# Optimization experiments

Hardware: AMD Instinct MI355X
Metric: run time of the kernel (lower is better)

The kernel has to match this reference:

```python
import jax, jax.numpy as jnp
import numpy as np

B, H = 8192, 768


def _mk_linear(key, fan_in, fan_out):
    k1, k2 = jax.random.split(key)
    lim = 1.0 / np.sqrt(fan_in)
    W = jax.random.uniform(k1, (fan_out, fan_in), jnp.float32, -lim, lim)
    b = jax.random.uniform(k2, (fan_out,), jnp.float32, -lim, lim)
    return W, b


def setup_inputs() -> dict:
    key = jax.random.key(0)
    ks = jax.random.split(key, 6)
    modal_a = jax.random.normal(ks[0], (B, H), jnp.float32)
    modal_b = jax.random.normal(ks[1], (B, H), jnp.float32)
    W1m, b1m = _mk_linear(ks[2], H, H)
    W2m, b2m = _mk_linear(ks[3], H, H)
    W1v, b1v = _mk_linear(ks[4], H, H)
    W2v, b2v = _mk_linear(ks[5], H, H)
    return {"modal_a": modal_a, "modal_b": modal_b,
            "W1m": W1m, "b1m": b1m, "W2m": W2m, "b2m": b2m,
            "W1v": W1v, "b1v": b1v, "W2v": W2v, "b2v": b2v}


def reference(modal_a, modal_b, W1m, b1m, W2m, b2m, W1v, b1v, W2v, b2v):
    # mlp_mu: Linear -> Tanh -> Linear
    mu = jnp.tanh(modal_a @ W1m.T + b1m) @ W2m.T + b2m              # [B,H]
    # mlp_logvar: Linear -> Tanh -> Linear -> Tanh
    logvar = jnp.tanh(jnp.tanh(modal_a @ W1v.T + b1v) @ W2v.T + b2v)  # [B,H]
    inv_var = jnp.exp(-logvar)

    positive = -(mu - modal_b) ** 2 * 0.5 * inv_var                  # [B,H]

    # mean_j (mu[j] - mu[i])^2 = E[mu^2] - 2*mu[i]*E[mu] + mu[i]^2  (per feature dim)
    # Algebraic reduction of the O(B^2*H) tile in the original code.
    mu_mean = jnp.mean(mu, axis=0)                                   # [H]
    mu_sq_mean = jnp.mean(mu * mu, axis=0)                           # [H]
    pair_sq = mu_sq_mean - 2.0 * mu * mu_mean + mu * mu              # [B,H]
    negative = -pair_sq * 0.5 * inv_var                              # [B,H]

    pos_sum = jnp.sum(positive, axis=-1)                             # [B]
    neg_sum = jnp.sum(negative, axis=-1)                             # [B]
    lld = jnp.mean(pos_sum)
    bound = jnp.mean(pos_sum - neg_sum)
    return (lld, bound)
```

## Files before the change

### kernel.cpp

```cpp
#include <hip/hip_runtime.h>
#include <hip/hip_fp8.h>
#include <math.h>

typedef float v4f __attribute__((ext_vector_type(4)));

static constexpr int Bn = 8192;
static constexpr int Hn = 768;
static constexpr float invB = 1.0f / 8192.0f;

__device__ __forceinline__ unsigned char cvt_e4m3(float x) {
    __hip_fp8_e4m3 t(x);
    return t.__x;
}

__device__ __forceinline__ float fast_tanh(float x) {
    float xc = fminf(fmaxf(x, -15.0f), 15.0f);
    float e = __expf(2.0f * xc);
    float r = __builtin_amdgcn_rcpf(e + 1.0f);
    return 1.0f - 2.0f * r;
}

__global__ void prep_kernel(const float* __restrict__ A,
                            const float* __restrict__ W1m, const float* __restrict__ W2m,
                            const float* __restrict__ W1v, const float* __restrict__ W2v,
                            unsigned char* __restrict__ A_f8,
                            unsigned char* __restrict__ W1m_f8, unsigned char* __restrict__ W2m_f8,
                            unsigned char* __restrict__ W1v_f8, unsigned char* __restrict__ W2v_f8,
                            float* __restrict__ zbuf, int nzero) {
    const int tid = blockIdx.x * blockDim.x + threadIdx.x;
    if (tid < nzero) zbuf[tid] = 0.0f;
    constexpr int A4 = Bn * Hn / 4;
    constexpr int W4 = Hn * Hn / 4;
    const int total = A4 + 4 * W4;
    const int stride = gridDim.x * blockDim.x;
    for (int i = tid; i < total; i += stride) {
        const float* s; unsigned char* d; int j;
        if (i < A4) { s = A; d = A_f8; j = i; }
        else {
            int k = i - A4; int w = k / W4; j = k - w * W4;
            s = (w == 0) ? W1m : (w == 1) ? W2m : (w == 2) ? W1v : W2v;
            d = (w == 0) ? W1m_f8 : (w == 1) ? W2m_f8 : (w == 2) ? W1v_f8 : W2v_f8;
        }
        float4 v = ((const float4*)s)[j];
        unsigned p = (unsigned)cvt_e4m3(v.x)
                   | ((unsigned)cvt_e4m3(v.y) << 8)
                   | ((unsigned)cvt_e4m3(v.z) << 16)
                   | ((unsigned)cvt_e4m3(v.w) << 24);
        ((unsigned*)d)[j] = p;
    }
}


__launch_bounds__(512, 2)
__global__ void gemm_l1(const unsigned char* __restrict__ A_g,
                        const unsigned char* __restrict__ Wm_g, const unsigned char* __restrict__ Wv_g,
                        const float* __restrict__ bm, const float* __restrict__ bv,
                        unsigned char* __restrict__ outm, unsigned char* __restrict__ outv) {
    __shared__ __align__(16) unsigned char As[64 * 768];
    const int t = threadIdx.x;
    const int strip0 = blockIdx.x * 64;
    const int br = blockIdx.y;
    const unsigned char* __restrict__ Wg = br ? Wv_g : Wm_g;
    const float* __restrict__ bias = br ? bv : bm;
    unsigned char* __restrict__ out = br ? outv : outm;

    {
        const int row = t >> 3, c8 = t & 7;
        const unsigned char* src = A_g + (size_t)(strip0 + row) * Hn + c8 * 16;
        unsigned char* dst = As + row * 768;
#pragma unroll
        for (int j = 0; j < 6; ++j) {
            const int c = c8 + 8 * j;
            uint4 v = *(const uint4*)(src + j * 128);
            *(uint4*)(dst + ((c ^ (row & 7)) << 4)) = v;
        }
    }
    __syncthreads();

    const int w = t >> 6, lane = t & 63;
    const int lr = lane & 15, quad = lane >> 4;
    const int wc0 = w * 96;

    const unsigned char* __restrict__ pW = Wg + (size_t)(wc0 + lr) * Hn + quad * 16;

    v4f acc[6][4] = {};
    ulonglong2 Wf[2][6], Af[2][4];

#define L1_LOADS(s_, ms_) do {                                                              \
    _Pragma("unroll")                                                                       \
    for (int ct = 0; ct < 6; ++ct)                                                          \
        Wf[s_][ct] = *(const ulonglong2*)(pW + ct * (16 * Hn) + (ms_) * 64);                \
    _Pragma("unroll")                                                                       \
    for (int rt = 0; rt < 4; ++rt) {                                                        \
        const int row_ = rt * 16 + lr;                                                      \
        const int slot_ = ((ms_) * 4 + quad) ^ (row_ & 7);                                  \
        Af[s_][rt] = *(const ulonglong2*)&As[row_ * 768 + slot_ * 16];                      \
    } } while (0)

#define L1_MFMA(s_) do {                                                                    \
    _Pragma("unroll")                                                                       \
    for (int ct = 0; ct < 6; ++ct)                                                          \
    _Pragma("unroll")                                                                       \
    for (int rt = 0; rt < 4; ++rt) {                                                        \
        acc[ct][rt] = __builtin_amdgcn_mfma_f32_16x16x32_fp8_fp8((long)Wf[s_][ct].x, (long)Af[s_][rt].x, acc[ct][rt], 0, 0, 0); \
        acc[ct][rt] = __builtin_amdgcn_mfma_f32_16x16x32_fp8_fp8((long)Wf[s_][ct].y, (long)Af[s_][rt].y, acc[ct][rt], 0, 0, 0); \
    } } while (0)

    L1_LOADS(0, 0);
#pragma unroll
    for (int ms = 0; ms < 12; ++ms) {
        if (ms < 11) {
            if ((ms & 1) == 0) L1_LOADS(1, ms + 1); else L1_LOADS(0, ms + 1);
        }
        if ((ms & 1) == 0) L1_MFMA(0); else L1_MFMA(1);
    }
#undef L1_LOADS
#undef L1_MFMA

    __syncthreads();
#pragma unroll
    for (int ct = 0; ct < 6; ++ct) {
        const float4 bb = *(const float4*)&bias[wc0 + ct * 16 + quad * 4];
        const int c = w * 6 + ct;
#pragma unroll
        for (int rt = 0; rt < 4; ++rt) {
            const int row = rt * 16 + lr;
            v4f a = acc[ct][rt];
            unsigned p = (unsigned)cvt_e4m3(fast_tanh(a[0] + bb.x))
                       | ((unsigned)cvt_e4m3(fast_tanh(a[1] + bb.y)) << 8)
                       | ((unsigned)cvt_e4m3(fast_tanh(a[2] + bb.z)) << 16)
                       | ((unsigned)cvt_e4m3(fast_tanh(a[3] + bb.w)) << 24);
            *(unsigned*)&As[row * 768 + ((c ^ (row & 7)) << 4) + quad * 4] = p;
        }
    }
    __syncthreads();
#pragma unroll
    for (int i = 0; i < 6; ++i) {
        const int u = i * 512 + t;
        const int row = u / 48, c = u - row * 48;
        uint4 v = *(const uint4*)&As[row * 768 + ((c ^ (row & 7)) << 4)];
        *(uint4*)&out[(size_t)(strip0 + row) * Hn + c * 16] = v;
    }
}

__device__ __forceinline__ void l2_gemm(const unsigned char* Hsrc, const unsigned char* pW,
                                        int lr, int quad, v4f acc[2][6]) {
    ulonglong2 Wf[2][6], Af[2][2];
#define L2_LOADS(s_, ms_) do {                                                              \
    _Pragma("unroll")                                                                       \
    for (int ct = 0; ct < 6; ++ct)                                                          \
        Wf[s_][ct] = *(const ulonglong2*)(pW + ct * (16 * Hn) + (ms_) * 64);                \
    _Pragma("unroll")                                                                       \
    for (int rt = 0; rt < 2; ++rt) {                                                        \
        const int row_ = rt * 16 + lr;                                                      \
        const int slot_ = ((ms_) * 4 + quad) ^ (row_ & 7);                                  \
        Af[s_][rt] = *(const ulonglong2*)&Hsrc[row_ * 768 + slot_ * 16];                    \
    } } while (0)

#define L2_MFMA(s_) do {                                                                    \
    _Pragma("unroll")                                                                       \
    for (int rt = 0; rt < 2; ++rt)                                                          \
    _Pragma("unroll")                                                                       \
    for (int ct = 0; ct < 6; ++ct) {                                                        \
        acc[rt][ct] = __builtin_amdgcn_mfma_f32_16x16x32_fp8_fp8((long)Af[s_][rt].x, (long)Wf[s_][ct].x, acc[rt][ct], 0, 0, 0); \
        acc[rt][ct] = __builtin_amdgcn_mfma_f32_16x16x32_fp8_fp8((long)Af[s_][rt].y, (long)Wf[s_][ct].y, acc[rt][ct], 0, 0, 0); \
    } } while (0)

    L2_LOADS(0, 0);
#pragma unroll
    for (int ms = 0; ms < 12; ++ms) {
        if (ms < 11) {
            if ((ms & 1) == 0) L2_LOADS(1, ms + 1); else L2_LOADS(0, ms + 1);
        }
        if ((ms & 1) == 0) L2_MFMA(0); else L2_MFMA(1);
    }
#undef L2_LOADS
#undef L2_MFMA
}

__launch_bounds__(512, 2)
__global__ void gemm_l2(const unsigned char* __restrict__ h1m_g, const unsigned char* __restrict__ h1v_g,
                        const unsigned char* __restrict__ Wm_g, const unsigned char* __restrict__ Wv_g,
                        const float* __restrict__ bm, const float* __restrict__ bv,
                        const float* __restrict__ mb,
                        float* __restrict__ cs, float* __restrict__ cs2,
                        float* __restrict__ siv, float* __restrict__ sivmu,
                        float* __restrict__ accum, float* __restrict__ outp) {
    __shared__ __align__(16) unsigned char Hs[2][32 * 768];
    const int t = threadIdx.x;
    const int strip0 = blockIdx.x * 32;

    {
        const int row = t >> 4, c16 = t & 15;
        const size_t goff = (size_t)(strip0 + row) * Hn + c16 * 16;
#pragma unroll
        for (int b = 0; b < 2; ++b) {
            const unsigned char* src = (b ? h1v_g : h1m_g) + goff;
            unsigned char* dst = Hs[b] + row * 768;
#pragma unroll
            for (int j = 0; j < 3; ++j) {
                const int c = c16 + 16 * j;
                uint4 v = *(const uint4*)(src + j * 256);
                *(uint4*)(dst + ((c ^ (row & 7)) << 4)) = v;
            }
        }
    }
    __syncthreads();

    const int w = t >> 6, lane = t & 63;
    const int lr = lane & 15, quad = lane >> 4;
    const int wc0 = w * 96;

    v4f am[2][6] = {}, av[2][6] = {};

    l2_gemm(&Hs[0][0], Wm_g + (size_t)(wc0 + lr) * Hn + quad * 16, lr, quad, am);
    l2_gemm(&Hs[1][0], Wv_g + (size_t)(wc0 + lr) * Hn + quad * 16, lr, quad, av);

    float pos = 0.f, q = 0.f;
#pragma unroll
    for (int ct = 0; ct < 6; ++ct) {
        const int col = wc0 + ct * 16 + lr;
        const float bmc = bm[col], bvc = bv[col];
        float c1 = 0.f, c2 = 0.f, c3 = 0.f, c4 = 0.f;
#pragma unroll
        for (int rt = 0; rt < 2; ++rt) {
#pragma unroll
            for (int r = 0; r < 4; ++r) {
                const int row = strip0 + rt * 16 + quad * 4 + r;
                float mu = am[rt][ct][r] + bmc;
                float tv = fast_tanh(av[rt][ct][r] + bvc);
                float iv = __expf(-tv);
                float mbv = mb[(size_t)row * Hn + col];
                float d = mu - mbv;
                pos += iv * d * d;
                q   += iv * mu * mu;
                c1 += mu; c2 += mu * mu; c3 += iv; c4 += iv * mu;
            }
        }
        c1 += __shfl_xor(c1, 16); c1 += __shfl_xor(c1, 32);
        c2 += __shfl_xor(c2, 16); c2 += __shfl_xor(c2, 32);
        c3 += __shfl_xor(c3, 16); c3 += __shfl_xor(c3, 32);
        c4 += __shfl_xor(c4, 16); c4 += __shfl_xor(c4, 32);
        if (quad == 0) {
            atomicAdd(&cs[col], c1);
            atomicAdd(&cs2[col], c2);
            atomicAdd(&siv[col], c3);
            atomicAdd(&sivmu[col], c4);
        }
    }
    for (int off = 32; off > 0; off >>= 1) {
        pos += __shfl_down(pos, off);
        q   += __shfl_down(q, off);
    }
    __shared__ float redP[8], redQ[8];
    if (lane == 0) { redP[w] = pos; redQ[w] = q; }
    __syncthreads();
    __shared__ int is_last;
    if (t == 0) {
        float sp = 0.f, sq = 0.f;
#pragma unroll
        for (int i = 0; i < 8; ++i) { sp += redP[i]; sq += redQ[i]; }
        atomicAdd(&accum[0], sp);
        atomicAdd(&accum[1], sq);
        __threadfence();
        unsigned old = atomicAdd((unsigned int*)&accum[3], 1u);
        is_last = (old == gridDim.x * gridDim.y - 1) ? 1 : 0;
    }
    __syncthreads();
    if (is_last) {
        float term = 0.f;
        for (int h = t; h < Hn; h += 512) {
            float v1 = atomicAdd(&cs[h], 0.0f);
            float v2 = atomicAdd(&cs2[h], 0.0f);
            float v3 = atomicAdd(&siv[h], 0.0f);
            float v4 = atomicAdd(&sivmu[h], 0.0f);
            term += v3 * v2 - 2.0f * v4 * v1;
        }
        for (int off = 32; off > 0; off >>= 1) term += __shfl_down(term, off);
        __shared__ float redT[8];
        if (lane == 0) redT[w] = term;
        __syncthreads();
        if (t == 0) {
            float T = 0.f;
#pragma unroll
            for (int i = 0; i < 8; ++i) T += redT[i];
            float P = atomicAdd(&accum[0], 0.0f);
            float Q = atomicAdd(&accum[1], 0.0f);
            float pos_sum = -0.5f * P;
            float neg_sum = -0.5f * (T * invB + Q);
            outp[0] = pos_sum * invB;
            outp[1] = (pos_sum - neg_sum) * invB;
        }
    }
}

extern "C" void kernel_launch(void* const* d_in, const int* in_sizes, int n_in,
                              void* d_out, int out_size, void* d_ws, size_t ws_size,
                              hipStream_t stream) {
    const float* modal_a = (const float*)d_in[0];
    const float* modal_b = (const float*)d_in[1];
    const float* W1m = (const float*)d_in[2];
    const float* b1m = (const float*)d_in[3];
    const float* W2m = (const float*)d_in[4];
    const float* b2m = (const float*)d_in[5];
    const float* W1v = (const float*)d_in[6];
    const float* b1v = (const float*)d_in[7];
    const float* W2v = (const float*)d_in[8];
    const float* b2v = (const float*)d_in[9];
    float* out = (float*)d_out;

    char* ws = (char*)d_ws;
    constexpr size_t szA8 = (size_t)Bn * Hn;
    constexpr size_t szW8 = (size_t)Hn * Hn;
    unsigned char* A_f8   = (unsigned char*)(ws);
    unsigned char* h1m_f8 = (unsigned char*)(ws + szA8);
    unsigned char* h1v_f8 = (unsigned char*)(ws + 2 * szA8);
    unsigned char* W1m_f8 = (unsigned char*)(ws + 3 * szA8);
    unsigned char* W2m_f8 = (unsigned char*)(ws + 3 * szA8 + szW8);
    unsigned char* W1v_f8 = (unsigned char*)(ws + 3 * szA8 + 2 * szW8);
    unsigned char* W2v_f8 = (unsigned char*)(ws + 3 * szA8 + 3 * szW8);
    float* cs     = (float*)(ws + 3 * szA8 + 4 * szW8);
    float* cs2    = cs + Hn;
    float* siv    = cs + 2 * Hn;
    float* sivmu  = cs + 3 * Hn;
    float* accum  = cs + 4 * Hn;

    prep_kernel<<<1280, 256, 0, stream>>>(modal_a, W1m, W2m, W1v, W2v,
                                          A_f8, W1m_f8, W2m_f8, W1v_f8, W2v_f8,
                                          cs, 4 * Hn + 8);

    gemm_l1<<<dim3(Bn / 64, 2), 512, 0, stream>>>(
        A_f8, W1m_f8, W1v_f8, b1m, b1v, h1m_f8, h1v_f8);

    gemm_l2<<<dim3(Bn / 32), 512, 0, stream>>>(
        h1m_f8, h1v_f8, W2m_f8, W2v_f8, b2m, b2v, modal_b,
        cs, cs2, siv, sivmu, accum, out);
}
```

Before: 190.2 us.

## Fuse both MLP layers and input FP8 conversion into one kernel per row strip

Merges the layer-1 GEMM, the layer-2 GEMM and the epilogue into a single kernel working on 32-row strips. The fp32 input is converted to FP8 directly into shared memory and the hidden activations stay in shared memory, so the FP8 copy of A and the h1 round trips through global memory are gone. The mu and logvar branches now share each A fragment load. The prep kernel only converts weights. In exchange each block reloads all four weight matrices, holds more accumulator registers, and uses a wider 16-way XOR swizzle.

Measured after the change: 189.9 us. Within noise of the previous version (-0.1%).

```diff
diff --git a/kernel.cpp b/kernel.cpp
--- a/kernel.cpp
+++ b/kernel.cpp
@@ -11,6 +11,13 @@
 __device__ __forceinline__ unsigned char cvt_e4m3(float x) {
     __hip_fp8_e4m3 t(x);
     return t.__x;
+}
+
+__device__ __forceinline__ unsigned pack4_e4m3(float4 f) {
+    return (unsigned)cvt_e4m3(f.x)
+         | ((unsigned)cvt_e4m3(f.y) << 8)
+         | ((unsigned)cvt_e4m3(f.z) << 16)
+         | ((unsigned)cvt_e4m3(f.w) << 24);
 }
 
 __device__ __forceinline__ float fast_tanh(float x) {
@@ -20,59 +27,54 @@
     return 1.0f - 2.0f * r;
 }
 
-__global__ void prep_kernel(const float* __restrict__ A,
-                            const float* __restrict__ W1m, const float* __restrict__ W2m,
-                            const float* __restrict__ W1v, const float* __restrict__ W2v,
-                            unsigned char* __restrict__ A_f8,
-                            unsigned char* __restrict__ W1m_f8, unsigned char* __restrict__ W2m_f8,
-                            unsigned char* __restrict__ W1v_f8, unsigned char* __restrict__ W2v_f8,
-                            float* __restrict__ zbuf, int nzero) {
+__global__ void prep_w(const float* __restrict__ W1m, const float* __restrict__ W2m,
+                       const float* __restrict__ W1v, const float* __restrict__ W2v,
+                       unsigned char* __restrict__ W1m_f8, unsigned char* __restrict__ W2m_f8,
+                       unsigned char* __restrict__ W1v_f8, unsigned char* __restrict__ W2v_f8,
+                       float* __restrict__ zbuf, int nzero) {
     const int tid = blockIdx.x * blockDim.x + threadIdx.x;
     if (tid < nzero) zbuf[tid] = 0.0f;
-    constexpr int A4 = Bn * Hn / 4;
     constexpr int W4 = Hn * Hn / 4;
-    const int total = A4 + 4 * W4;
+    const int total = 4 * W4;
     const int stride = gridDim.x * blockDim.x;
     for (int i = tid; i < total; i += stride) {
-        const float* s; unsigned char* d; int j;
-        if (i < A4) { s = A; d = A_f8; j = i; }
-        else {
-            int k = i - A4; int w = k / W4; j = k - w * W4;
-            s = (w == 0) ? W1m : (w == 1) ? W2m : (w == 2) ? W1v : W2v;
-            d = (w == 0) ? W1m_f8 : (w == 1) ? W2m_f8 : (w == 2) ? W1v_f8 : W2v_f8;
-        }
+        int w = i / W4, j = i - w * W4;
+        const float* s = (w == 0) ? W1m : (w == 1) ? W2m : (w == 2) ? W1v : W2v;
+        unsigned char* d = (w == 0) ? W1m_f8 : (w == 1) ? W2m_f8 : (w == 2) ? W1v_f8 : W2v_f8;
         float4 v = ((const float4*)s)[j];
-        unsigned p = (unsigned)cvt_e4m3(v.x)
-                   | ((unsigned)cvt_e4m3(v.y) << 8)
-                   | ((unsigned)cvt_e4m3(v.z) << 16)
-                   | ((unsigned)cvt_e4m3(v.w) << 24);
-        ((unsigned*)d)[j] = p;
-    }
-}
-
+        ((unsigned*)d)[j] = pack4_e4m3(v);
+    }
+}
 
 __launch_bounds__(512, 2)
-__global__ void gemm_l1(const unsigned char* __restrict__ A_g,
-                        const unsigned char* __restrict__ Wm_g, const unsigned char* __restrict__ Wv_g,
-                        const float* __restrict__ bm, const float* __restrict__ bv,
-                        unsigned char* __restrict__ outm, unsigned char* __restrict__ outv) {
-    __shared__ __align__(16) unsigned char As[64 * 768];
+__global__ void club_fused(const float* __restrict__ A_g,
+                           const unsigned char* __restrict__ W1m, const unsigned char* __restrict__ W1v,
+                           const unsigned char* __restrict__ W2m, const unsigned char* __restrict__ W2v,
+                           const float* __restrict__ b1m, const float* __restrict__ b1v,
+                           const float* __restrict__ b2m, const float* __restrict__ b2v,
+                           const float* __restrict__ mb,
+                           float* __restrict__ cs, float* __restrict__ cs2,
+                           float* __restrict__ siv, float* __restrict__ sivmu,
+                           float* __restrict__ accum, float* __restrict__ outp) {
+    __shared__ __align__(16) unsigned char Hm[32 * 768];
+    __shared__ __align__(16) unsigned char Xs[32 * 768];
     const int t = threadIdx.x;
-    const int strip0 = blockIdx.x * 64;
-    const int br = blockIdx.y;
-    const unsigned char* __restrict__ Wg = br ? Wv_g : Wm_g;
-    const float* __restrict__ bias = br ? bv : bm;
-    unsigned char* __restrict__ out = br ? outv : outm;
+    const int strip0 = blockIdx.x * 32;
 
     {
-        const int row = t >> 3, c8 = t & 7;
-        const unsigned char* src = A_g + (size_t)(strip0 + row) * Hn + c8 * 16;
-        unsigned char* dst = As + row * 768;
-#pragma unroll
-        for (int j = 0; j < 6; ++j) {
-            const int c = c8 + 8 * j;
-            uint4 v = *(const uint4*)(src + j * 128);
-            *(uint4*)(dst + ((c ^ (row & 7)) << 4)) = v;
+        const int row = t >> 4, seg = t & 15;
+        const float* src = A_g + (size_t)(strip0 + row) * Hn;
+#pragma unroll
+        for (int j = 0; j < 3; ++j) {
+            const int c = seg + 16 * j;
+            float4 f0 = *(const float4*)(src + c * 16 + 0);
+            float4 f1 = *(const float4*)(src + c * 16 + 4);
+            float4 f2 = *(const float4*)(src + c * 16 + 8);
+            float4 f3 = *(const float4*)(src + c * 16 + 12);
+            uint4 p;
+            p.x = pack4_e4m3(f0); p.y = pack4_e4m3(f1);
+            p.z = pack4_e4m3(f2); p.w = pack4_e4m3(f3);
+            *(uint4*)&Xs[row * 768 + ((c ^ (row & 15)) << 4)] = p;
         }
     }
     __syncthreads();
@@ -81,154 +83,132 @@
     const int lr = lane & 15, quad = lane >> 4;
     const int wc0 = w * 96;
 
-    const unsigned char* __restrict__ pW = Wg + (size_t)(wc0 + lr) * Hn + quad * 16;
-
-    v4f acc[6][4] = {};
-    ulonglong2 Wf[2][6], Af[2][4];
-
-#define L1_LOADS(s_, ms_) do {                                                              \
-    _Pragma("unroll")                                                                       \
-    for (int ct = 0; ct < 6; ++ct)                                                          \
-        Wf[s_][ct] = *(const ulonglong2*)(pW + ct * (16 * Hn) + (ms_) * 64);                \
-    _Pragma("unroll")                                                                       \
-    for (int rt = 0; rt < 4; ++rt) {                                                        \
-        const int row_ = rt * 16 + lr;                                                      \
-        const int slot_ = ((ms_) * 4 + quad) ^ (row_ & 7);                                  \
-        Af[s_][rt] = *(const ulonglong2*)&As[row_ * 768 + slot_ * 16];                      \
+    v4f am[6][2] = {}, av[6][2] = {};
+    {
+        ulonglong2 Wm1[2][6], Wv1[2][6];
+        const unsigned char* __restrict__ pWm = W1m + (size_t)(wc0 + lr) * Hn + quad * 16;
+        const unsigned char* __restrict__ pWv = W1v + (size_t)(wc0 + lr) * Hn + quad * 16;
+
+#define LDW1(s_, ms_) do {                                                                  \
+    _Pragma("unroll")                                                                       \
+    for (int ct = 0; ct < 6; ++ct) {                                                        \
+        Wm1[s_][ct] = *(const ulonglong2*)(pWm + ct * (16 * Hn) + (ms_) * 64);              \
+        Wv1[s_][ct] = *(const ulonglong2*)(pWv + ct * (16 * Hn) + (ms_) * 64);              \
     } } while (0)
 
-#define L1_MFMA(s_) do {                                                                    \
-    _Pragma("unroll")                                                                       \
-    for (int ct = 0; ct < 6; ++ct)                                                          \
-    _Pragma("unroll")                                                                       \
-    for (int rt = 0; rt < 4; ++rt) {                                                        \
-        acc[ct][rt] = __builtin_amdgcn_mfma_f32_16x16x32_fp8_fp8((long)Wf[s_][ct].x, (long)Af[s_][rt].x, acc[ct][rt], 0, 0, 0); \
-        acc[ct][rt] = __builtin_amdgcn_mfma_f32_16x16x32_fp8_fp8((long)Wf[s_][ct].y, (long)Af[s_][rt].y, acc[ct][rt], 0, 0, 0); \
-    } } while (0)
-
-    L1_LOADS(0, 0);
-#pragma unroll
-    for (int ms = 0; ms < 12; ++ms) {
-        if (ms < 11) {
-            if ((ms & 1) == 0) L1_LOADS(1, ms + 1); else L1_LOADS(0, ms + 1);
-        }
-        if ((ms & 1) == 0) L1_MFMA(0); else L1_MFMA(1);
-    }
-#undef L1_LOADS
-#undef L1_MFMA
-
-    __syncthreads();
-#pragma unroll
-    for (int ct = 0; ct < 6; ++ct) {
-        const float4 bb = *(const float4*)&bias[wc0 + ct * 16 + quad * 4];
-        const int c = w * 6 + ct;
-#pragma unroll
-        for (int rt = 0; rt < 4; ++rt) {
-            const int row = rt * 16 + lr;
-            v4f a = acc[ct][rt];
-            unsigned p = (unsigned)cvt_e4m3(fast_tanh(a[0] + bb.x))
-                       | ((unsigned)cvt_e4m3(fast_tanh(a[1] + bb.y)) << 8)
-                       | ((unsigned)cvt_e4m3(fast_tanh(a[2] + bb.z)) << 16)
-                       | ((unsigned)cvt_e4m3(fast_tanh(a[3] + bb.w)) << 24);
-            *(unsigned*)&As[row * 768 + ((c ^ (row & 7)) << 4) + quad * 4] = p;
-        }
-    }
-    __syncthreads();
-#pragma unroll
-    for (int i = 0; i < 6; ++i) {
-        const int u = i * 512 + t;
-        const int row = u / 48, c = u - row * 48;
-        uint4 v = *(const uint4*)&As[row * 768 + ((c ^ (row & 7)) << 4)];
-        *(uint4*)&out[(size_t)(strip0 + row) * Hn + c * 16] = v;
-    }
-}
-
-__device__ __forceinline__ void l2_gemm(const unsigned char* Hsrc, const unsigned char* pW,
-                                        int lr, int quad, v4f acc[2][6]) {
-    ulonglong2 Wf[2][6], Af[2][2];
-#define L2_LOADS(s_, ms_) do {                                                              \
-    _Pragma("unroll")                                                                       \
-    for (int ct = 0; ct < 6; ++ct)                                                          \
-        Wf[s_][ct] = *(const ulonglong2*)(pW + ct * (16 * Hn) + (ms_) * 64);                \
+#define FM1(s_, ms_) do {                                                                   \
+    ulonglong2 Af[2];                                                                       \
     _Pragma("unroll")                                                                       \
     for (int rt = 0; rt < 2; ++rt) {                                                        \
         const int row_ = rt * 16 + lr;                                                      \
-        const int slot_ = ((ms_) * 4 + quad) ^ (row_ & 7);                                  \
-        Af[s_][rt] = *(const ulonglong2*)&Hsrc[row_ * 768 + slot_ * 16];                    \
+        const int k_ = (ms_) * 4 + quad;                                                    \
+        Af[rt] = *(const ulonglong2*)&Xs[row_ * 768 + ((k_ ^ (row_ & 15)) << 4)];           \
+    }                                                                                       \
+    _Pragma("unroll")                                                                       \
+    for (int ct = 0; ct < 6; ++ct)                                                          \
+    _Pragma("unroll")                                                                       \
+    for (int rt = 0; rt < 2; ++rt) {                                                        \
+        am[ct][rt] = __builtin_amdgcn_mfma_f32_16x16x32_fp8_fp8((long)Wm1[s_][ct].x, (long)Af[rt].x, am[ct][rt], 0, 0, 0); \
+        am[ct][rt] = __builtin_amdgcn_mfma_f32_16x16x32_fp8_fp8((long)Wm1[s_][ct].y, (long)Af[rt].y, am[ct][rt], 0, 0, 0); \
+        av[ct][rt] = __builtin_amdgcn_mfma_f32_16x16x32_fp8_fp8((long)Wv1[s_][ct].x, (long)Af[rt].x, av[ct][rt], 0, 0, 0); \
+        av[ct][rt] = __builtin_amdgcn_mfma_f32_16x16x32_fp8_fp8((long)Wv1[s_][ct].y, (long)Af[rt].y, av[ct][rt], 0, 0, 0); \
     } } while (0)
 
-#define L2_MFMA(s_) do {                                                                    \
+        LDW1(0, 0);
+#pragma unroll
+        for (int ms = 0; ms < 11; ++ms) {
+            if ((ms & 1) == 0) { LDW1(1, ms + 1); FM1(0, ms); }
+            else               { LDW1(0, ms + 1); FM1(1, ms); }
+        }
+        FM1(1, 11);
+#undef LDW1
+#undef FM1
+    }
+
+    __syncthreads();
+
+#pragma unroll
+    for (int ct = 0; ct < 6; ++ct) {
+        const float4 bbm = *(const float4*)&b1m[wc0 + ct * 16 + quad * 4];
+        const float4 bbv = *(const float4*)&b1v[wc0 + ct * 16 + quad * 4];
+        const int cc = w * 6 + ct;
+#pragma unroll
+        for (int rt = 0; rt < 2; ++rt) {
+            const int row = rt * 16 + lr;
+            v4f a = am[ct][rt];
+            unsigned pm = (unsigned)cvt_e4m3(fast_tanh(a[0] + bbm.x))
+                        | ((unsigned)cvt_e4m3(fast_tanh(a[1] + bbm.y)) << 8)
+                        | ((unsigned)cvt_e4m3(fast_tanh(a[2] + bbm.z)) << 16)
+                        | ((unsigned)cvt_e4m3(fast_tanh(a[3] + bbm.w)) << 24);
+            v4f b = av[ct][rt];
+            unsigned pv = (unsigned)cvt_e4m3(fast_tanh(b[0] + bbv.x))
+                        | ((unsigned)cvt_e4m3(fast_tanh(b[1] + bbv.y)) << 8)
+                        | ((unsigned)cvt_e4m3(fast_tanh(b[2] + bbv.z)) << 16)
+                        | ((unsigned)cvt_e4m3(fast_tanh(b[3] + bbv.w)) << 24);
+            const int off = row * 768 + ((cc ^ (row & 15)) << 4) + quad * 4;
+            *(unsigned*)&Hm[off] = pm;
+            *(unsigned*)&Xs[off] = pv;
+        }
+    }
+    __syncthreads();
+
+    v4f cm[2][6] = {}, cv[2][6] = {};
+    {
+        ulonglong2 Wm2[2][6], Wv2[2][6];
+        const unsigned char* __restrict__ pWm = W2m + (size_t)(wc0 + lr) * Hn + quad * 16;
+        const unsigned char* __restrict__ pWv = W2v + (size_t)(wc0 + lr) * Hn + quad * 16;
+
+#define LDW2(s_, ms_) do {                                                                  \
+    _Pragma("unroll")                                                                       \
+    for (int ct = 0; ct < 6; ++ct) {                                                        \
+        Wm2[s_][ct] = *(const ulonglong2*)(pWm + ct * (16 * Hn) + (ms_) * 64);              \
+        Wv2[s_][ct] = *(const ulonglong2*)(pWv + ct * (16 * Hn) + (ms_) * 64);              \
+    } } while (0)
+
+#define FM2(s_, ms_) do {                                                                   \
+    ulonglong2 Am[2], Av[2];                                                                \
+    _Pragma("unroll")                                                                       \
+    for (int rt = 0; rt < 2; ++rt) {                                                        \
+        const int row_ = rt * 16 + lr;                                                      \
+        const int k_ = (ms_) * 4 + quad;                                                    \
+        const int off_ = row_ * 768 + ((k_ ^ (row_ & 15)) << 4);                            \
+        Am[rt] = *(const ulonglong2*)&Hm[off_];                                             \
+        Av[rt] = *(const ulonglong2*)&Xs[off_];                                             \
+    }                                                                                       \
     _Pragma("unroll")                                                                       \
     for (int rt = 0; rt < 2; ++rt)                                                          \
     _Pragma("unroll")                                                                       \
     for (int ct = 0; ct < 6; ++ct) {                                                        \
-        acc[rt][ct] = __builtin_amdgcn_mfma_f32_16x16x32_fp8_fp8((long)Af[s_][rt].x, (long)Wf[s_][ct].x, acc[rt][ct], 0, 0, 0); \
-        acc[rt][ct] = __builtin_amdgcn_mfma_f32_16x16x32_fp8_fp8((long)Af[s_][rt].y, (long)Wf[s_][ct].y, acc[rt][ct], 0, 0, 0); \
+        cm[rt][ct] = __builtin_amdgcn_mfma_f32_16x16x32_fp8_fp8((long)Am[rt].x, (long)Wm2[s_][ct].x, cm[rt][ct], 0, 0, 0); \
+        cm[rt][ct] = __builtin_amdgcn_mfma_f32_16x16x32_fp8_fp8((long)Am[rt].y, (long)Wm2[s_][ct].y, cm[rt][ct], 0, 0, 0); \
+        cv[rt][ct] = __builtin_amdgcn_mfma_f32_16x16x32_fp8_fp8((long)Av[rt].x, (long)Wv2[s_][ct].x, cv[rt][ct], 0, 0, 0); \
+        cv[rt][ct] = __builtin_amdgcn_mfma_f32_16x16x32_fp8_fp8((long)Av[rt].y, (long)Wv2[s_][ct].y, cv[rt][ct], 0, 0, 0); \
     } } while (0)
 
-    L2_LOADS(0, 0);
-#pragma unroll
-    for (int ms = 0; ms < 12; ++ms) {
-        if (ms < 11) {
-            if ((ms & 1) == 0) L2_LOADS(1, ms + 1); else L2_LOADS(0, ms + 1);
-        }
-        if ((ms & 1) == 0) L2_MFMA(0); else L2_MFMA(1);
-    }
-#undef L2_LOADS
-#undef L2_MFMA
-}
-
-__launch_bounds__(512, 2)
-__global__ void gemm_l2(const unsigned char* __restrict__ h1m_g, const unsigned char* __restrict__ h1v_g,
-                        const unsigned char* __restrict__ Wm_g, const unsigned char* __restrict__ Wv_g,
-                        const float* __restrict__ bm, const float* __restrict__ bv,
-                        const float* __restrict__ mb,
-                        float* __restrict__ cs, float* __restrict__ cs2,
-                        float* __restrict__ siv, float* __restrict__ sivmu,
-                        float* __restrict__ accum, float* __restrict__ outp) {
-    __shared__ __align__(16) unsigned char Hs[2][32 * 768];
-    const int t = threadIdx.x;
-    const int strip0 = blockIdx.x * 32;
-
-    {
-        const int row = t >> 4, c16 = t & 15;
-        const size_t goff = (size_t)(strip0 + row) * Hn + c16 * 16;
-#pragma unroll
-        for (int b = 0; b < 2; ++b) {
-            const unsigned char* src = (b ? h1v_g : h1m_g) + goff;
-            unsigned char* dst = Hs[b] + row * 768;
-#pragma unroll
-            for (int j = 0; j < 3; ++j) {
-                const int c = c16 + 16 * j;
-                uint4 v = *(const uint4*)(src + j * 256);
-                *(uint4*)(dst + ((c ^ (row & 7)) << 4)) = v;
-            }
-        }
-    }
-    __syncthreads();
-
-    const int w = t >> 6, lane = t & 63;
-    const int lr = lane & 15, quad = lane >> 4;
-    const int wc0 = w * 96;
-
-    v4f am[2][6] = {}, av[2][6] = {};
-
-    l2_gemm(&Hs[0][0], Wm_g + (size_t)(wc0 + lr) * Hn + quad * 16, lr, quad, am);
-    l2_gemm(&Hs[1][0], Wv_g + (size_t)(wc0 + lr) * Hn + quad * 16, lr, quad, av);
+        LDW2(0, 0);
+#pragma unroll
+        for (int ms = 0; ms < 11; ++ms) {
+            if ((ms & 1) == 0) { LDW2(1, ms + 1); FM2(0, ms); }
+            else               { LDW2(0, ms + 1); FM2(1, ms); }
+        }
+        FM2(1, 11);
+#undef LDW2
+#undef FM2
+    }
 
     float pos = 0.f, q = 0.f;
 #pragma unroll
     for (int ct = 0; ct < 6; ++ct) {
         const int col = wc0 + ct * 16 + lr;
-        const float bmc = bm[col], bvc = bv[col];
+        const float bmc = b2m[col], bvc = b2v[col];
         float c1 = 0.f, c2 = 0.f, c3 = 0.f, c4 = 0.f;
 #pragma unroll
         for (int rt = 0; rt < 2; ++rt) {
 #pragma unroll
             for (int r = 0; r < 4; ++r) {
                 const int row = strip0 + rt * 16 + quad * 4 + r;
-                float mu = am[rt][ct][r] + bmc;
-                float tv = fast_tanh(av[rt][ct][r] + bvc);
+                float mu = cm[rt][ct][r] + bmc;
+                float tv = fast_tanh(cv[rt][ct][r] + bvc);
                 float iv = __expf(-tv);
                 float mbv = mb[(size_t)row * Hn + col];
                 float d = mu - mbv;
@@ -264,7 +244,7 @@
         atomicAdd(&accum[1], sq);
         __threadfence();
         unsigned old = atomicAdd((unsigned int*)&accum[3], 1u);
-        is_last = (old == gridDim.x * gridDim.y - 1) ? 1 : 0;
+        is_last = (old == gridDim.x - 1) ? 1 : 0;
     }
     __syncthreads();
     if (is_last) {
@@ -310,29 +290,23 @@
     float* out = (float*)d_out;
 
     char* ws = (char*)d_ws;
-    constexpr size_t szA8 = (size_t)Bn * Hn;
     constexpr size_t szW8 = (size_t)Hn * Hn;
-    unsigned char* A_f8   = (unsigned char*)(ws);
-    unsigned char* h1m_f8 = (unsigned char*)(ws + szA8);
-    unsigned char* h1v_f8 = (unsigned char*)(ws + 2 * szA8);
-    unsigned char* W1m_f8 = (unsigned char*)(ws + 3 * szA8);
-    unsigned char* W2m_f8 = (unsigned char*)(ws + 3 * szA8 + szW8);
-    unsigned char* W1v_f8 = (unsigned char*)(ws + 3 * szA8 + 2 * szW8);
-    unsigned char* W2v_f8 = (unsigned char*)(ws + 3 * szA8 + 3 * szW8);
-    float* cs     = (float*)(ws + 3 * szA8 + 4 * szW8);
+    unsigned char* W1m_f8 = (unsigned char*)(ws);
+    unsigned char* W2m_f8 = (unsigned char*)(ws + szW8);
+    unsigned char* W1v_f8 = (unsigned char*)(ws + 2 * szW8);
+    unsigned char* W2v_f8 = (unsigned char*)(ws + 3 * szW8);
+    float* cs     = (float*)(ws + 4 * szW8);
     float* cs2    = cs + Hn;
     float* siv    = cs + 2 * Hn;
     float* sivmu  = cs + 3 * Hn;
     float* accum  = cs + 4 * Hn;
 
-    prep_kernel<<<1280, 256, 0, stream>>>(modal_a, W1m, W2m, W1v, W2v,
-                                          A_f8, W1m_f8, W2m_f8, W1v_f8, W2v_f8,
-                                          cs, 4 * Hn + 8);
-
-    gemm_l1<<<dim3(Bn / 64, 2), 512, 0, stream>>>(
-        A_f8, W1m_f8, W1v_f8, b1m, b1v, h1m_f8, h1v_f8);
-
-    gemm_l2<<<dim3(Bn / 32), 512, 0, stream>>>(
-        h1m_f8, h1v_f8, W2m_f8, W2v_f8, b2m, b2v, modal_b,
+    prep_w<<<576, 256, 0, stream>>>(W1m, W2m, W1v, W2v,
+                                    W1m_f8, W2m_f8, W1v_f8, W2v_f8,
+                                    cs, 4 * Hn + 8);
+
+    club_fused<<<dim3(Bn / 32), 512, 0, stream>>>(
+        modal_a, W1m_f8, W1v_f8, W2m_f8, W2v_f8,
+        b1m, b1v, b2m, b2v, modal_b,
         cs, cs2, siv, sivmu, accum, out);
 }
```
